# Performance work log

Hardware: AMD Instinct MI355X
Metric: run time of the kernel (lower is better)

Reference implementation:

```python
import jax, jax.numpy as jnp
import numpy as np

B, T, C = 4, 2048, 1024
H, D = 16, 64  # num_heads, head_dim
P = 64         # prefix length


def setup_inputs() -> dict:
    key = jax.random.key(0)
    ks = jax.random.split(key, 12)
    s = 1.0 / np.sqrt(C)
    return {
        "x": jax.random.normal(ks[0], (B, T, C), dtype=jnp.float32),
        "attn_mask": jax.random.randint(ks[1], (B, 1, 1, T), 0, 2, dtype=jnp.int32),
        "prefix_k": jax.random.normal(ks[2], (B, H, P, D), dtype=jnp.float32),
        "prefix_v": jax.random.normal(ks[3], (B, H, P, D), dtype=jnp.float32),
        "Wq": jax.random.normal(ks[4], (C, C), dtype=jnp.float32) * s,
        "bq": jnp.zeros((C,), dtype=jnp.float32),
        "Wk": jax.random.normal(ks[5], (C, C), dtype=jnp.float32) * s,
        "bk": jnp.zeros((C,), dtype=jnp.float32),
        "Wv": jax.random.normal(ks[6], (C, C), dtype=jnp.float32) * s,
        "bv": jnp.zeros((C,), dtype=jnp.float32),
        "Wo": jax.random.normal(ks[7], (C, C), dtype=jnp.float32) * s,
        "bo": jnp.zeros((C,), dtype=jnp.float32),
    }


def _heads(y):
    # [B,T,C] -> [B,H,T,D]
    return y.reshape(B, T, H, D).transpose(0, 2, 1, 3)


def reference(x, attn_mask, prefix_k, prefix_v, Wq, bq, Wk, bk, Wv, bv, Wo, bo):
    q = _heads(x @ Wq.T + bq)
    k = _heads(x @ Wk.T + bk)
    v = _heads(x @ Wv.T + bv)
    # concat prefix K/V along key dim -> [B,H,P+T,D]
    k = jnp.concatenate([prefix_k, k], axis=2)
    v = jnp.concatenate([prefix_v, v], axis=2)
    # prefix positions are always visible
    prefix_mask = jnp.ones((B, 1, 1, P), dtype=attn_mask.dtype)
    mask = jnp.concatenate([prefix_mask, attn_mask], axis=-1)  # [B,1,1,P+T]
    scores = jnp.einsum('bhtd,bhsd->bhts', q, k) / jnp.sqrt(jnp.asarray(D, x.dtype))
    scores = jnp.where(mask == 0, -jnp.inf, scores)
    w = jax.nn.softmax(scores, axis=-1)
    o = jnp.einsum('bhts,bhsd->bhtd', w, v)
    o = o.transpose(0, 2, 1, 3).reshape(B, T, C)
    return o @ Wo.T + bo
```

## Files before the change

kernel.cpp:

```cpp
#include <hip/hip_runtime.h>
#include <hip/hip_bf16.h>

typedef __bf16 bf16;
typedef __attribute__((ext_vector_type(8))) __bf16 bf16x8;
typedef __attribute__((ext_vector_type(4))) __bf16 bf16x4;
typedef __attribute__((ext_vector_type(4))) float f32x4;
typedef __attribute__((ext_vector_type(16))) float f32x16;

#define MFMA16(a, b, c) __builtin_amdgcn_mfma_f32_16x16x32_bf16(a, b, c, 0, 0, 0)
#define MFMA32(a, b, c) __builtin_amdgcn_mfma_f32_32x32x16_bf16(a, b, c, 0, 0, 0)

__device__ __forceinline__ void gl_lds16(const void* g, void* l) {
    __builtin_amdgcn_global_load_lds(
        (const __attribute__((address_space(1))) void*)g,
        (__attribute__((address_space(3))) void*)l, 16, 0, 0);
}

#define QSCALE 0.18033688011f
#define LOGBIAS 24.0f

__global__ __launch_bounds__(256) void prep(
    const float* __restrict__ x, const float* __restrict__ Wq,
    const float* __restrict__ Wk, const float* __restrict__ Wv,
    const float* __restrict__ Wo, const float* __restrict__ pk,
    const float* __restrict__ pv, const int* __restrict__ mask,
    bf16* __restrict__ xb, bf16* __restrict__ wb,
    bf16* __restrict__ k_ws, bf16* __restrict__ vt_ws,
    int* __restrict__ ridx, int* __restrict__ nkv)
{
    const int blk = blockIdx.x, tid = threadIdx.x;
    if (blk < 4) {
        const int b = blk, lane = tid & 63, wv = tid >> 6;
        const int* mb = mask + b * 2048;
        int loc[8], s = 0;
#pragma unroll
        for (int e = 0; e < 8; ++e) { loc[e] = (mb[tid * 8 + e] != 0); s += loc[e]; }
        int inc = s;
#pragma unroll
        for (int off = 1; off < 64; off <<= 1) {
            int t = __shfl_up(inc, off);
            if (lane >= off) inc += t;
        }
        __shared__ int wt[4];
        if (lane == 63) wt[wv] = inc;
        __syncthreads();
        int wo = 0;
        for (int w = 0; w < wv; ++w) wo += wt[w];
        int excl = wo + inc - s;
#pragma unroll
        for (int e = 0; e < 8; ++e) {
            if (loc[e]) ridx[b * 2048 + excl] = tid * 8 + e;
            excl += loc[e];
        }
        if (tid == 255) nkv[b] = 64 + wo + inc;
    } else if (blk < 260) {
        int i = (blk - 4) * 256 + tid;
        {
            int base = i * 4;
            int bh = base >> 12, rem = base & 4095;
            float4 a = *(const float4*)&pk[base];
            bf16x4 ab;
            ab[0] = (bf16)a.x; ab[1] = (bf16)a.y; ab[2] = (bf16)a.z; ab[3] = (bf16)a.w;
            *(bf16x4*)&k_ws[(size_t)bh * (2112 * 64) + rem] = ab;
        }
        {
            int bh = i >> 10, r = i & 1023;
            int d = r >> 4, sq = (r & 15) * 4;
            bf16x4 vb;
#pragma unroll
            for (int e = 0; e < 4; ++e)
                vb[e] = (bf16)pv[(size_t)bh * 4096 + (sq + e) * 64 + d];
            *(bf16x4*)&vt_ws[((size_t)bh * 64 + d) * 2112 + sq] = vb;
        }
    } else {
        int i4 = (blk - 260) * 256 + tid;
        const float* src; bf16* dst; int off;
        if (i4 < 2097152) { src = x; dst = xb; off = i4; }
        else {
            int j = i4 - 2097152;
            int sel = j >> 18;
            off = j & 262143;
            src = (sel == 0) ? Wq : (sel == 1) ? Wk : (sel == 2) ? Wv : Wo;
            dst = wb + (size_t)sel * 1048576;
        }
        float4 a = *(const float4*)&src[(size_t)off * 4];
        bf16x4 o;
        o[0] = (bf16)a.x; o[1] = (bf16)a.y; o[2] = (bf16)a.z; o[3] = (bf16)a.w;
        *(bf16x4*)&dst[(size_t)off * 4] = o;
    }
}

__global__ __launch_bounds__(256) void proj_gemm(
    const bf16* __restrict__ X, const bf16* __restrict__ Wb,
    const float* __restrict__ bq, const float* __restrict__ bk,
    const float* __restrict__ bv, const int* __restrict__ ridx,
    const int* __restrict__ nkv,
    bf16* __restrict__ q_ws, bf16* __restrict__ k_ws, bf16* __restrict__ vt_ws)
{
    const int bx = blockIdx.x;
    int kind, m0 = 0, n0, bsel = 0, nvis = 0, mbase = 0;
    const bf16* W;
    const float* bias;
    if (bx < 512) {
        kind = 0; m0 = (bx >> 3) * 128; n0 = (bx & 7) * 128;
        W = Wb; bias = bq;
    } else {
        int j = bx - 512;
        kind = 1 + (j >> 9);
        int r = j & 511;
        bsel = r >> 7;
        mbase = ((r & 127) >> 3) * 128;
        n0 = (r & 7) * 128;
        nvis = nkv[bsel] - 64;
        if (mbase >= nvis) return;
        W = Wb + (size_t)kind * 1048576;
        bias = (kind == 1) ? bk : bv;
    }

    __shared__ bf16 As[128 * 32];
    __shared__ bf16 Bs[128 * 32];
    const int tid = threadIdx.x, lane = tid & 63, wave = tid >> 6;
    const int ln = lane & 15, quad = lane >> 4;
    const int wr = (wave >> 1) * 64, wc = (wave & 1) * 64;
    const int srow = wave * 32 + (lane >> 2);
    const int scol = (lane & 3) * 8;

    const bf16 *Xr0, *Xr1;
    if (kind == 0) {
        Xr0 = X + (size_t)(m0 + srow) * 1024 + scol;
        Xr1 = Xr0 + (size_t)16 * 1024;
    } else {
        int g0 = mbase + srow, g1 = g0 + 16;
        int c0 = (g0 < nvis) ? g0 : nvis - 1;
        int c1 = (g1 < nvis) ? g1 : nvis - 1;
        Xr0 = X + (size_t)(bsel * 2048 + ridx[bsel * 2048 + c0]) * 1024 + scol;
        Xr1 = X + (size_t)(bsel * 2048 + ridx[bsel * 2048 + c1]) * 1024 + scol;
    }

    const f32x4 z4 = {0.f, 0.f, 0.f, 0.f};
    f32x4 acc[4][4];
#pragma unroll
    for (int i = 0; i < 4; ++i)
#pragma unroll
        for (int j = 0; j < 4; ++j) acc[i][j] = z4;

    for (int k0 = 0; k0 < 1024; k0 += 32) {
        __syncthreads();
        gl_lds16(Xr0 + k0, &As[(wave * 32) * 32]);
        gl_lds16(Xr1 + k0, &As[(wave * 32 + 16) * 32]);
        gl_lds16(&W[(size_t)(n0 + srow) * 1024 + k0 + scol],      &Bs[(wave * 32) * 32]);
        gl_lds16(&W[(size_t)(n0 + srow + 16) * 1024 + k0 + scol], &Bs[(wave * 32 + 16) * 32]);
        __syncthreads();
        bf16x8 af[4], bfr[4];
#pragma unroll
        for (int i = 0; i < 4; ++i) af[i]  = *(const bf16x8*)&As[(wr + i * 16 + ln) * 32 + quad * 8];
#pragma unroll
        for (int j = 0; j < 4; ++j) bfr[j] = *(const bf16x8*)&Bs[(wc + j * 16 + ln) * 32 + quad * 8];
#pragma unroll
        for (int i = 0; i < 4; ++i)
#pragma unroll
            for (int j = 0; j < 4; ++j)
                acc[i][j] = MFMA16(af[i], bfr[j], acc[i][j]);
    }

    if (kind == 0) {
#pragma unroll
        for (int j = 0; j < 4; ++j) {
            const int n = n0 + wc + j * 16 + ln;
            const float bb = bias[n];
            const int h = n >> 6, d = n & 63;
#pragma unroll
            for (int i = 0; i < 4; ++i) {
                int m = m0 + wr + i * 16 + quad * 4;
                int b = m >> 11, t = m & 2047;
#pragma unroll
                for (int r = 0; r < 4; ++r)
                    q_ws[((size_t)(b * 16 + h) * 2048 + t + r) * 64 + d] =
                        (bf16)((acc[i][j][r] + bb) * QSCALE);
            }
        }
    } else {
#pragma unroll
        for (int j = 0; j < 4; ++j) {
            const int n = n0 + wc + j * 16 + ln;
            const float bb = bias[n];
            const int h = n >> 6, d = n & 63;
            const size_t bh64 = (size_t)(bsel * 16 + h);
#pragma unroll
            for (int i = 0; i < 4; ++i) {
                int ml = mbase + wr + i * 16 + quad * 4;
                if (kind == 1) {
#pragma unroll
                    for (int r = 0; r < 4; ++r)
                        if (ml + r < nvis)
                            k_ws[(bh64 * 2112 + 64 + ml + r) * 64 + d] =
                                (bf16)(acc[i][j][r] + bb);
                } else {
                    if (ml + 3 < nvis) {
                        bf16x4 pb;
#pragma unroll
                        for (int r = 0; r < 4; ++r) pb[r] = (bf16)(acc[i][j][r] + bb);
                        *(bf16x4*)&vt_ws[(bh64 * 64 + d) * 2112 + 64 + ml] = pb;
                    } else {
#pragma unroll
                        for (int r = 0; r < 4; ++r)
                            if (ml + r < nvis)
                                vt_ws[(bh64 * 64 + d) * 2112 + 64 + ml + r] =
                                    (bf16)(acc[i][j][r] + bb);
                    }
                }
            }
        }
    }
}

__global__ __launch_bounds__(256) void attn_kernel(
    const bf16* __restrict__ Q, const bf16* __restrict__ K,
    const bf16* __restrict__ VT, const int* __restrict__ nk,
    bf16* __restrict__ O)
{
    __shared__ bf16 smem[128 * 72];
    bf16* Ks = smem;
    bf16* Vt = smem + 64 * 72;
    const int tid = threadIdx.x, wave = tid >> 6, lane = tid & 63;
    const int ln = lane & 31, hh = lane >> 5;
    const int bh = blockIdx.y, b = bh >> 4, head = bh & 15;
    const bf16* __restrict__ Kb  = K  + (size_t)bh * (2112 * 64);
    const bf16* __restrict__ Vtb = VT + (size_t)bh * (64 * 2112);
    const int qg = blockIdx.x * 128 + wave * 32 + ln;
    const int nkeys = nk[b];
    const int send = ((nkeys + 63) >> 6) << 6;

    bf16x8 qf[4];
#pragma unroll
    for (int kt = 0; kt < 4; ++kt)
        qf[kt] = *(const bf16x8*)&Q[((size_t)bh * 2048 + qg) * 64 + kt * 16 + hh * 8];

    float l_r = 0.f;
    f32x16 acc[2];
#pragma unroll
    for (int r = 0; r < 16; ++r) { acc[0][r] = 0.f; acc[1][r] = 0.f; }

    const int ks_s = tid >> 3, ks_c = (tid & 7) * 8;
    const int vd = tid >> 3, v8 = tid & 7, vs = v8 * 8;
    const int vcb = (v8 >> 1) * 16 + ((v8 & 1) ? 4 : 0);

    bf16x8 kr0, kr1, vr0, vr1;
    kr0 = *(const bf16x8*)&Kb[(size_t)ks_s * 64 + ks_c];
    kr1 = *(const bf16x8*)&Kb[(size_t)(ks_s + 32) * 64 + ks_c];
    vr0 = *(const bf16x8*)&Vtb[(size_t)vd * 2112 + vs];
    vr1 = *(const bf16x8*)&Vtb[(size_t)(vd + 32) * 2112 + vs];

    for (int s0 = 0; s0 < send; s0 += 64) {
        __syncthreads();
        *(bf16x8*)&Ks[ks_s * 72 + ks_c]        = kr0;
        *(bf16x8*)&Ks[(ks_s + 32) * 72 + ks_c] = kr1;
        {
            bf16x4 lo, hi;
#pragma unroll
            for (int e = 0; e < 4; ++e) { lo[e] = vr0[e]; hi[e] = vr0[4 + e]; }
            *(bf16x4*)&Vt[vd * 72 + vcb]     = lo;
            *(bf16x4*)&Vt[vd * 72 + vcb + 8] = hi;
#pragma unroll
            for (int e = 0; e < 4; ++e) { lo[e] = vr1[e]; hi[e] = vr1[4 + e]; }
            *(bf16x4*)&Vt[(vd + 32) * 72 + vcb]     = lo;
            *(bf16x4*)&Vt[(vd + 32) * 72 + vcb + 8] = hi;
        }
        __syncthreads();

        if (s0 + 64 < send) {
            const int sn = s0 + 64;
            kr0 = *(const bf16x8*)&Kb[(size_t)(sn + ks_s) * 64 + ks_c];
            kr1 = *(const bf16x8*)&Kb[(size_t)(sn + ks_s + 32) * 64 + ks_c];
            vr0 = *(const bf16x8*)&Vtb[(size_t)vd * 2112 + sn + vs];
            vr1 = *(const bf16x8*)&Vtb[(size_t)(vd + 32) * 2112 + sn + vs];
        }

        f32x16 sc[2];
#pragma unroll
        for (int ts = 0; ts < 2; ++ts) {
            f32x16 s16;
#pragma unroll
            for (int r = 0; r < 16; ++r) s16[r] = 0.f;
#pragma unroll
            for (int kt = 0; kt < 4; ++kt) {
                bf16x8 kf = *(const bf16x8*)&Ks[(ts * 32 + ln) * 72 + kt * 16 + hh * 8];
                s16 = MFMA32(kf, qf[kt], s16);
            }
            sc[ts] = s16;
        }

        float rs = 0.f;
        bf16x8 pf[4];
        if (s0 + 64 <= nkeys) {
#pragma unroll
            for (int ts = 0; ts < 2; ++ts)
#pragma unroll
                for (int rg = 0; rg < 4; ++rg)
#pragma unroll
                    for (int i = 0; i < 4; ++i) {
                        float p = __builtin_amdgcn_exp2f(sc[ts][rg * 4 + i] - LOGBIAS);
                        rs += p;
                        pf[ts * 2 + (rg >> 1)][(rg & 1) * 4 + i] = (bf16)p;
                    }
        } else {
#pragma unroll
            for (int ts = 0; ts < 2; ++ts)
#pragma unroll
                for (int rg = 0; rg < 4; ++rg)
#pragma unroll
                    for (int i = 0; i < 4; ++i) {
                        int key = s0 + ts * 32 + rg * 8 + hh * 4 + i;
                        float add = (key < nkeys) ? -LOGBIAS : -1e30f;
                        float p = __builtin_amdgcn_exp2f(sc[ts][rg * 4 + i] + add);
                        rs += p;
                        pf[ts * 2 + (rg >> 1)][(rg & 1) * 4 + i] = (bf16)p;
                    }
        }
        l_r += rs;

#pragma unroll
        for (int st = 0; st < 4; ++st) {
            bf16x8 a0 = *(const bf16x8*)&Vt[ln * 72 + st * 16 + hh * 8];
            acc[0] = MFMA32(a0, pf[st], acc[0]);
            bf16x8 a1 = *(const bf16x8*)&Vt[(32 + ln) * 72 + st * 16 + hh * 8];
            acc[1] = MFMA32(a1, pf[st], acc[1]);
        }
    }

    __syncthreads();
    l_r += __shfl_xor(l_r, 32);
    float inv = 1.0f / l_r;
    bf16* scratch = smem + wave * (32 * 72);
#pragma unroll
    for (int td = 0; td < 2; ++td)
#pragma unroll
        for (int rg = 0; rg < 4; ++rg) {
            bf16x4 ob;
#pragma unroll
            for (int i = 0; i < 4; ++i) ob[i] = (bf16)(acc[td][rg * 4 + i] * inv);
            *(bf16x4*)&scratch[ln * 72 + td * 32 + rg * 8 + hh * 4] = ob;
        }
    __builtin_amdgcn_s_waitcnt(0xC07F);
    const int orow = lane >> 3, oc = (lane & 7) * 8;
#pragma unroll
    for (int pass = 0; pass < 4; ++pass) {
        int ml = pass * 8 + orow;
        bf16x8 ov = *(const bf16x8*)&scratch[ml * 72 + oc];
        int qrow = blockIdx.x * 128 + wave * 32 + ml;
        *(bf16x8*)&O[((size_t)b * 2048 + qrow) * 1024 + head * 64 + oc] = ov;
    }
}

__global__ __launch_bounds__(256) void out_proj_gemm(
    const bf16* __restrict__ A, const bf16* __restrict__ W,
    const float* __restrict__ bias, float* __restrict__ out)
{
    __shared__ bf16 As[128 * 32];
    __shared__ bf16 Bs[128 * 32];
    const int m0 = blockIdx.x * 128, n0 = blockIdx.y * 128;
    const int tid = threadIdx.x, lane = tid & 63, wave = tid >> 6;
    const int ln = lane & 15, quad = lane >> 4;
    const int wr = (wave >> 1) * 64, wc = (wave & 1) * 64;
    const int srow = wave * 32 + (lane >> 2);
    const int scol = (lane & 3) * 8;

    const f32x4 z4 = {0.f, 0.f, 0.f, 0.f};
    f32x4 acc[4][4];
#pragma unroll
    for (int i = 0; i < 4; ++i)
#pragma unroll
        for (int j = 0; j < 4; ++j) acc[i][j] = z4;

    for (int k0 = 0; k0 < 1024; k0 += 32) {
        __syncthreads();
        gl_lds16(&A[(size_t)(m0 + srow) * 1024 + k0 + scol],      &As[(wave * 32) * 32]);
        gl_lds16(&A[(size_t)(m0 + srow + 16) * 1024 + k0 + scol], &As[(wave * 32 + 16) * 32]);
        gl_lds16(&W[(size_t)(n0 + srow) * 1024 + k0 + scol],      &Bs[(wave * 32) * 32]);
        gl_lds16(&W[(size_t)(n0 + srow + 16) * 1024 + k0 + scol], &Bs[(wave * 32 + 16) * 32]);
        __syncthreads();
        bf16x8 af[4], bfr[4];
#pragma unroll
        for (int i = 0; i < 4; ++i) af[i]  = *(const bf16x8*)&As[(wr + i * 16 + ln) * 32 + quad * 8];
#pragma unroll
        for (int j = 0; j < 4; ++j) bfr[j] = *(const bf16x8*)&Bs[(wc + j * 16 + ln) * 32 + quad * 8];
#pragma unroll
        for (int i = 0; i < 4; ++i)
#pragma unroll
            for (int j = 0; j < 4; ++j)
                acc[i][j] = MFMA16(af[i], bfr[j], acc[i][j]);
    }

#pragma unroll
    for (int j = 0; j < 4; ++j) {
        const int n = n0 + wc + j * 16 + ln;
        const float bb = bias[n];
#pragma unroll
        for (int i = 0; i < 4; ++i) {
#pragma unroll
            for (int r = 0; r < 4; ++r) {
                int m = m0 + wr + i * 16 + quad * 4 + r;
                out[(size_t)m * 1024 + n] = acc[i][j][r] + bb;
            }
        }
    }
}

extern "C" void kernel_launch(void* const* d_in, const int* in_sizes, int n_in,
                              void* d_out, int out_size, void* d_ws, size_t ws_size,
                              hipStream_t stream)
{
    const float* x    = (const float*)d_in[0];
    const int*   mask = (const int*)d_in[1];
    const float* pk   = (const float*)d_in[2];
    const float* pv   = (const float*)d_in[3];
    const float* Wq   = (const float*)d_in[4];
    const float* bq   = (const float*)d_in[5];
    const float* Wk   = (const float*)d_in[6];
    const float* bk   = (const float*)d_in[7];
    const float* Wv   = (const float*)d_in[8];
    const float* bv   = (const float*)d_in[9];
    const float* Wo   = (const float*)d_in[10];
    const float* bo   = (const float*)d_in[11];
    float* out = (float*)d_out;

    bf16* xb    = (bf16*)d_ws;
    bf16* wb    = xb + (size_t)8388608;
    bf16* q_ws  = wb + (size_t)4194304;
    bf16* k_ws  = q_ws + (size_t)8388608;
    bf16* vt_ws = k_ws + (size_t)8650752;
    int*  ridx  = (int*)(vt_ws + (size_t)8650752);
    int*  nkv   = ridx + 4 * 2048;
    bf16* a_ws  = xb;

    prep<<<dim3(12548), 256, 0, stream>>>(x, Wq, Wk, Wv, Wo, pk, pv, mask,
                                          xb, wb, k_ws, vt_ws, ridx, nkv);
    proj_gemm<<<dim3(1536), 256, 0, stream>>>(xb, wb, bq, bk, bv, ridx, nkv,
                                              q_ws, k_ws, vt_ws);
    attn_kernel<<<dim3(16, 64), 256, 0, stream>>>(q_ws, k_ws, vt_ws, nkv, a_ws);
    out_proj_gemm<<<dim3(64, 8), 256, 0, stream>>>(a_ws, wb + (size_t)3 * 1048576,
                                                   bo, out);
}
```

Measured before the change: 256.2 us.

## Rewrite projection GEMMs as double-buffered 256x128 pipelined tiles with swizzled LDS

Both the QKV projection and output projection GEMMs now share a new device routine that uses 256x128 tiles, 8 waves, a BK=64 double-buffered LDS ring, XOR-swizzled LDS columns to avoid bank conflicts, and split global prefetches interleaved with MFMA phases under setprio. Block indices are remapped so consecutive blocks spread across N tiles for better L2 reuse. The aim is to hide global-load latency and the barrier stalls of the old single-buffered 128x128 BK=32 loop. In exchange it uses 96KB of LDS per block and more barriers per iteration, and relies on hand-placed waitcnt counts being correct.

```diff
diff --git a/kernel.cpp b/kernel.cpp
--- a/kernel.cpp
+++ b/kernel.cpp
@@ -15,6 +15,9 @@
         (const __attribute__((address_space(1))) void*)g,
         (__attribute__((address_space(3))) void*)l, 16, 0, 0);
 }
+
+#define BARRIER() do { asm volatile("" ::: "memory"); \
+    __builtin_amdgcn_s_barrier(); asm volatile("" ::: "memory"); } while (0)
 
 #define QSCALE 0.18033688011f
 #define LOGBIAS 24.0f
@@ -90,52 +93,144 @@
     }
 }
 
-__global__ __launch_bounds__(256) void proj_gemm(
+__device__ __forceinline__ void gemm_pipe_256x128(
+    const bf16* a0, const bf16* a1, const bf16* a2, const bf16* a3,
+    const bf16* b0, const bf16* b1,
+    bf16* lds, const int wave, const int lane, f32x4 (&acc)[4][4])
+{
+    const int ln = lane & 15, quad = lane >> 4;
+    const int wm = wave >> 1, wn = wave & 1;
+    const int so = wave * 512;
+    const int aBase = (wm * 64 + ln) * 64;
+    const int bBase = 16384 + (wn * 64 + ln) * 64;
+    const int c0 = (quad * 8) ^ ((ln & 7) << 3);
+    const int c1 = (32 + quad * 8) ^ ((ln & 7) << 3);
+
+    gl_lds16(a0, lds + so);
+    gl_lds16(a1, lds + 4096 + so);
+    gl_lds16(a2, lds + 8192 + so);
+    gl_lds16(a3, lds + 12288 + so);
+    gl_lds16(b0, lds + 16384 + so);
+    gl_lds16(b1, lds + 20480 + so);
+
+#pragma unroll 2
+    for (int t = 0; t < 16; ++t) {
+        bf16* cur = lds + ((t & 1) ? 24576 : 0);
+        bf16* nxt = lds + ((t & 1) ? 0 : 24576);
+        const int kn = (t + 1) * 64;
+
+        if (t < 15) {
+            gl_lds16(a0 + kn, nxt + so);
+            gl_lds16(a1 + kn, nxt + 4096 + so);
+            gl_lds16(a2 + kn, nxt + 8192 + so);
+            asm volatile("s_waitcnt vmcnt(3)" ::: "memory");
+        } else {
+            asm volatile("s_waitcnt vmcnt(0)" ::: "memory");
+        }
+        BARRIER();
+
+        bf16x8 fa[4][2], fb[2][2];
+#pragma unroll
+        for (int mi = 0; mi < 4; ++mi) {
+            fa[mi][0] = *(const bf16x8*)(cur + aBase + mi * 1024 + c0);
+            fa[mi][1] = *(const bf16x8*)(cur + aBase + mi * 1024 + c1);
+        }
+#pragma unroll
+        for (int ni = 0; ni < 2; ++ni) {
+            fb[ni][0] = *(const bf16x8*)(cur + bBase + ni * 1024 + c0);
+            fb[ni][1] = *(const bf16x8*)(cur + bBase + ni * 1024 + c1);
+        }
+        __builtin_amdgcn_s_setprio(1);
+#pragma unroll
+        for (int mi = 0; mi < 4; ++mi)
+#pragma unroll
+            for (int ni = 0; ni < 2; ++ni) {
+                acc[mi][ni] = MFMA16(fa[mi][0], fb[ni][0], acc[mi][ni]);
+                acc[mi][ni] = MFMA16(fa[mi][1], fb[ni][1], acc[mi][ni]);
+            }
+        __builtin_amdgcn_s_setprio(0);
+        BARRIER();
+
+#pragma unroll
+        for (int ni = 0; ni < 2; ++ni) {
+            fb[ni][0] = *(const bf16x8*)(cur + bBase + (2 + ni) * 1024 + c0);
+            fb[ni][1] = *(const bf16x8*)(cur + bBase + (2 + ni) * 1024 + c1);
+        }
+        if (t < 15) {
+            gl_lds16(a3 + kn, nxt + 12288 + so);
+            gl_lds16(b0 + kn, nxt + 16384 + so);
+            gl_lds16(b1 + kn, nxt + 20480 + so);
+        }
+        BARRIER();
+        __builtin_amdgcn_s_setprio(1);
+#pragma unroll
+        for (int mi = 0; mi < 4; ++mi)
+#pragma unroll
+            for (int ni = 0; ni < 2; ++ni) {
+                acc[mi][2 + ni] = MFMA16(fa[mi][0], fb[ni][0], acc[mi][2 + ni]);
+                acc[mi][2 + ni] = MFMA16(fa[mi][1], fb[ni][1], acc[mi][2 + ni]);
+            }
+        __builtin_amdgcn_s_setprio(0);
+        BARRIER();
+    }
+}
+
+__global__ __launch_bounds__(512, 2) void proj_gemm(
     const bf16* __restrict__ X, const bf16* __restrict__ Wb,
     const float* __restrict__ bq, const float* __restrict__ bk,
     const float* __restrict__ bv, const int* __restrict__ ridx,
     const int* __restrict__ nkv,
     bf16* __restrict__ q_ws, bf16* __restrict__ k_ws, bf16* __restrict__ vt_ws)
 {
-    const int bx = blockIdx.x;
+    __shared__ bf16 lds[49152];
+    const int hw = blockIdx.x;
+    const int bx = (hw & 7) * 96 + (hw >> 3);
+    const int tid = threadIdx.x, wave = tid >> 6, lane = tid & 63;
+    const int sr8 = lane >> 3;
+    const int csw = ((lane & 7) ^ sr8) << 3;
+
     int kind, m0 = 0, n0, bsel = 0, nvis = 0, mbase = 0;
     const bf16* W;
     const float* bias;
-    if (bx < 512) {
-        kind = 0; m0 = (bx >> 3) * 128; n0 = (bx & 7) * 128;
+    if (bx < 256) {
+        kind = 0; m0 = (bx >> 3) * 256; n0 = (bx & 7) * 128;
         W = Wb; bias = bq;
     } else {
-        int j = bx - 512;
-        kind = 1 + (j >> 9);
-        int r = j & 511;
-        bsel = r >> 7;
-        mbase = ((r & 127) >> 3) * 128;
-        n0 = (r & 7) * 128;
+        int j = bx - 256;
+        kind = 1 + (j >> 8);
+        int r = j & 255;
+        bsel = r >> 6;
+        int rr = r & 63;
+        mbase = (rr >> 3) * 256;
+        n0 = (rr & 7) * 128;
         nvis = nkv[bsel] - 64;
         if (mbase >= nvis) return;
         W = Wb + (size_t)kind * 1048576;
         bias = (kind == 1) ? bk : bv;
     }
 
-    __shared__ bf16 As[128 * 32];
-    __shared__ bf16 Bs[128 * 32];
-    const int tid = threadIdx.x, lane = tid & 63, wave = tid >> 6;
-    const int ln = lane & 15, quad = lane >> 4;
-    const int wr = (wave >> 1) * 64, wc = (wave & 1) * 64;
-    const int srow = wave * 32 + (lane >> 2);
-    const int scol = (lane & 3) * 8;
-
-    const bf16 *Xr0, *Xr1;
+    const bf16 *a0, *a1, *a2, *a3;
     if (kind == 0) {
-        Xr0 = X + (size_t)(m0 + srow) * 1024 + scol;
-        Xr1 = Xr0 + (size_t)16 * 1024;
+        a0 = X + (size_t)(m0 + wave * 8 + sr8) * 1024 + csw;
+        a1 = a0 + (size_t)64 * 1024;
+        a2 = a0 + (size_t)128 * 1024;
+        a3 = a0 + (size_t)192 * 1024;
     } else {
-        int g0 = mbase + srow, g1 = g0 + 16;
-        int c0 = (g0 < nvis) ? g0 : nvis - 1;
-        int c1 = (g1 < nvis) ? g1 : nvis - 1;
-        Xr0 = X + (size_t)(bsel * 2048 + ridx[bsel * 2048 + c0]) * 1024 + scol;
-        Xr1 = X + (size_t)(bsel * 2048 + ridx[bsel * 2048 + c1]) * 1024 + scol;
-    }
+        const int* rb = ridx + bsel * 2048;
+        const int nv1 = nvis - 1;
+        int g = mbase + wave * 8 + sr8;
+        int e0 = (g       < nv1) ? g       : nv1;
+        int e1 = (g + 64  < nv1) ? g + 64  : nv1;
+        int e2 = (g + 128 < nv1) ? g + 128 : nv1;
+        int e3 = (g + 192 < nv1) ? g + 192 : nv1;
+        const bf16* Xb = X + (size_t)bsel * 2048 * 1024 + csw;
+        a0 = Xb + (size_t)rb[e0] * 1024;
+        a1 = Xb + (size_t)rb[e1] * 1024;
+        a2 = Xb + (size_t)rb[e2] * 1024;
+        a3 = Xb + (size_t)rb[e3] * 1024;
+    }
+    const bf16* b0 = W + (size_t)(n0 + wave * 8 + sr8) * 1024 + csw;
+    const bf16* b1 = b0 + (size_t)64 * 1024;
 
     const f32x4 z4 = {0.f, 0.f, 0.f, 0.f};
     f32x4 acc[4][4];
@@ -144,69 +239,54 @@
 #pragma unroll
         for (int j = 0; j < 4; ++j) acc[i][j] = z4;
 
-    for (int k0 = 0; k0 < 1024; k0 += 32) {
-        __syncthreads();
-        gl_lds16(Xr0 + k0, &As[(wave * 32) * 32]);
-        gl_lds16(Xr1 + k0, &As[(wave * 32 + 16) * 32]);
-        gl_lds16(&W[(size_t)(n0 + srow) * 1024 + k0 + scol],      &Bs[(wave * 32) * 32]);
-        gl_lds16(&W[(size_t)(n0 + srow + 16) * 1024 + k0 + scol], &Bs[(wave * 32 + 16) * 32]);
-        __syncthreads();
-        bf16x8 af[4], bfr[4];
-#pragma unroll
-        for (int i = 0; i < 4; ++i) af[i]  = *(const bf16x8*)&As[(wr + i * 16 + ln) * 32 + quad * 8];
-#pragma unroll
-        for (int j = 0; j < 4; ++j) bfr[j] = *(const bf16x8*)&Bs[(wc + j * 16 + ln) * 32 + quad * 8];
-#pragma unroll
-        for (int i = 0; i < 4; ++i)
-#pragma unroll
-            for (int j = 0; j < 4; ++j)
-                acc[i][j] = MFMA16(af[i], bfr[j], acc[i][j]);
-    }
-
+    gemm_pipe_256x128(a0, a1, a2, a3, b0, b1, lds, wave, lane, acc);
+
+    const int ln = lane & 15, quad = lane >> 4;
+    const int wm = wave >> 1, wn = wave & 1;
     if (kind == 0) {
 #pragma unroll
-        for (int j = 0; j < 4; ++j) {
-            const int n = n0 + wc + j * 16 + ln;
+        for (int ni = 0; ni < 4; ++ni) {
+            const int n = n0 + wn * 64 + ni * 16 + ln;
             const float bb = bias[n];
             const int h = n >> 6, d = n & 63;
 #pragma unroll
-            for (int i = 0; i < 4; ++i) {
-                int m = m0 + wr + i * 16 + quad * 4;
-                int b = m >> 11, t = m & 2047;
+            for (int mi = 0; mi < 4; ++mi) {
+                int m = m0 + wm * 64 + mi * 16 + quad * 4;
+                int b = m >> 11, tq = m & 2047;
 #pragma unroll
                 for (int r = 0; r < 4; ++r)
-                    q_ws[((size_t)(b * 16 + h) * 2048 + t + r) * 64 + d] =
-                        (bf16)((acc[i][j][r] + bb) * QSCALE);
+                    q_ws[((size_t)(b * 16 + h) * 2048 + tq + r) * 64 + d] =
+                        (bf16)((acc[mi][ni][r] + bb) * QSCALE);
             }
         }
     } else {
 #pragma unroll
-        for (int j = 0; j < 4; ++j) {
-            const int n = n0 + wc + j * 16 + ln;
+        for (int ni = 0; ni < 4; ++ni) {
+            const int n = n0 + wn * 64 + ni * 16 + ln;
             const float bb = bias[n];
             const int h = n >> 6, d = n & 63;
             const size_t bh64 = (size_t)(bsel * 16 + h);
 #pragma unroll
-            for (int i = 0; i < 4; ++i) {
-                int ml = mbase + wr + i * 16 + quad * 4;
+            for (int mi = 0; mi < 4; ++mi) {
+                int ml = mbase + wm * 64 + mi * 16 + quad * 4;
                 if (kind == 1) {
 #pragma unroll
                     for (int r = 0; r < 4; ++r)
                         if (ml + r < nvis)
                             k_ws[(bh64 * 2112 + 64 + ml + r) * 64 + d] =
-                                (bf16)(acc[i][j][r] + bb);
+                                (bf16)(acc[mi][ni][r] + bb);
                 } else {
                     if (ml + 3 < nvis) {
                         bf16x4 pb;
 #pragma unroll
-                        for (int r = 0; r < 4; ++r) pb[r] = (bf16)(acc[i][j][r] + bb);
+                        for (int r = 0; r < 4; ++r) pb[r] = (bf16)(acc[mi][ni][r] + bb);
                         *(bf16x4*)&vt_ws[(bh64 * 64 + d) * 2112 + 64 + ml] = pb;
                     } else {
 #pragma unroll
                         for (int r = 0; r < 4; ++r)
                             if (ml + r < nvis)
                                 vt_ws[(bh64 * 64 + d) * 2112 + 64 + ml + r] =
-                                    (bf16)(acc[i][j][r] + bb);
+                                    (bf16)(acc[mi][ni][r] + bb);
                     }
                 }
             }
@@ -352,18 +432,24 @@
     }
 }
 
-__global__ __launch_bounds__(256) void out_proj_gemm(
+__global__ __launch_bounds__(512, 2) void out_proj_gemm(
     const bf16* __restrict__ A, const bf16* __restrict__ W,
     const float* __restrict__ bias, float* __restrict__ out)
 {
-    __shared__ bf16 As[128 * 32];
-    __shared__ bf16 Bs[128 * 32];
-    const int m0 = blockIdx.x * 128, n0 = blockIdx.y * 128;
-    const int tid = threadIdx.x, lane = tid & 63, wave = tid >> 6;
-    const int ln = lane & 15, quad = lane >> 4;
-    const int wr = (wave >> 1) * 64, wc = (wave & 1) * 64;
-    const int srow = wave * 32 + (lane >> 2);
-    const int scol = (lane & 3) * 8;
+    __shared__ bf16 lds[49152];
+    const int hw = blockIdx.x;
+    const int bx = (hw & 7) * 32 + (hw >> 3);
+    const int m0 = (bx >> 3) * 256, n0 = (bx & 7) * 128;
+    const int tid = threadIdx.x, wave = tid >> 6, lane = tid & 63;
+    const int sr8 = lane >> 3;
+    const int csw = ((lane & 7) ^ sr8) << 3;
+
+    const bf16* a0 = A + (size_t)(m0 + wave * 8 + sr8) * 1024 + csw;
+    const bf16* a1 = a0 + (size_t)64 * 1024;
+    const bf16* a2 = a0 + (size_t)128 * 1024;
+    const bf16* a3 = a0 + (size_t)192 * 1024;
+    const bf16* b0 = W + (size_t)(n0 + wave * 8 + sr8) * 1024 + csw;
+    const bf16* b1 = b0 + (size_t)64 * 1024;
 
     const f32x4 z4 = {0.f, 0.f, 0.f, 0.f};
     f32x4 acc[4][4];
@@ -372,36 +458,20 @@
 #pragma unroll
         for (int j = 0; j < 4; ++j) acc[i][j] = z4;
 
-    for (int k0 = 0; k0 < 1024; k0 += 32) {
-        __syncthreads();
-        gl_lds16(&A[(size_t)(m0 + srow) * 1024 + k0 + scol],      &As[(wave * 32) * 32]);
-        gl_lds16(&A[(size_t)(m0 + srow + 16) * 1024 + k0 + scol], &As[(wave * 32 + 16) * 32]);
-        gl_lds16(&W[(size_t)(n0 + srow) * 1024 + k0 + scol],      &Bs[(wave * 32) * 32]);
-        gl_lds16(&W[(size_t)(n0 + srow + 16) * 1024 + k0 + scol], &Bs[(wave * 32 + 16) * 32]);
-        __syncthreads();
-        bf16x8 af[4], bfr[4];
-#pragma unroll
-        for (int i = 0; i < 4; ++i) af[i]  = *(const bf16x8*)&As[(wr + i * 16 + ln) * 32 + quad * 8];
-#pragma unroll
-        for (int j = 0; j < 4; ++j) bfr[j] = *(const bf16x8*)&Bs[(wc + j * 16 + ln) * 32 + quad * 8];
-#pragma unroll
-        for (int i = 0; i < 4; ++i)
-#pragma unroll
-            for (int j = 0; j < 4; ++j)
-                acc[i][j] = MFMA16(af[i], bfr[j], acc[i][j]);
-    }
-
-#pragma unroll
-    for (int j = 0; j < 4; ++j) {
-        const int n = n0 + wc + j * 16 + ln;
+    gemm_pipe_256x128(a0, a1, a2, a3, b0, b1, lds, wave, lane, acc);
+
+    const int ln = lane & 15, quad = lane >> 4;
+    const int wm = wave >> 1, wn = wave & 1;
+#pragma unroll
+    for (int ni = 0; ni < 4; ++ni) {
+        const int n = n0 + wn * 64 + ni * 16 + ln;
         const float bb = bias[n];
 #pragma unroll
-        for (int i = 0; i < 4; ++i) {
-#pragma unroll
-            for (int r = 0; r < 4; ++r) {
-                int m = m0 + wr + i * 16 + quad * 4 + r;
-                out[(size_t)m * 1024 + n] = acc[i][j][r] + bb;
-            }
+        for (int mi = 0; mi < 4; ++mi) {
+            int m = m0 + wm * 64 + mi * 16 + quad * 4;
+#pragma unroll
+            for (int r = 0; r < 4; ++r)
+                out[(size_t)(m + r) * 1024 + n] = acc[mi][ni][r] + bb;
         }
     }
 }
@@ -435,9 +505,9 @@
 
     prep<<<dim3(12548), 256, 0, stream>>>(x, Wq, Wk, Wv, Wo, pk, pv, mask,
                                           xb, wb, k_ws, vt_ws, ridx, nkv);
-    proj_gemm<<<dim3(1536), 256, 0, stream>>>(xb, wb, bq, bk, bv, ridx, nkv,
-                                              q_ws, k_ws, vt_ws);
+    proj_gemm<<<dim3(768), 512, 0, stream>>>(xb, wb, bq, bk, bv, ridx, nkv,
+                                             q_ws, k_ws, vt_ws);
     attn_kernel<<<dim3(16, 64), 256, 0, stream>>>(q_ws, k_ws, vt_ws, nkv, a_ws);
-    out_proj_gemm<<<dim3(64, 8), 256, 0, stream>>>(a_ws, wb + (size_t)3 * 1048576,
-                                                   bo, out);
-}
+    out_proj_gemm<<<dim3(256), 512, 0, stream>>>(a_ws, wb + (size_t)3 * 1048576,
+                                                 bo, out);
+}
```

New measurement: 252.1 us. About the same (-1.6%).
